# Kernel optimization log

Hardware: AMD Instinct MI355X
Metric: run time of the kernel (lower is better)

## Reference

```python
import jax, jax.numpy as jnp
import numpy as np

QUERY_DIM = 1024
CONTEXT_DIM = 768
HEADS = 16
DIM_HEAD = 64
INNER = HEADS * DIM_HEAD  # 1024
SCALE = DIM_HEAD ** -0.5


def setup_inputs() -> dict:
    key = jax.random.key(0)
    ks = jax.random.split(key, 8)
    b, nq, nkv = 4, 2048, 1024
    x = jax.random.normal(ks[0], (b, nq, QUERY_DIM), dtype=jnp.float32)
    context = jax.random.normal(ks[1], (b, nkv, CONTEXT_DIM), dtype=jnp.float32)
    mask = jax.random.randint(ks[2], (b, nkv), 0, 2).astype(jnp.bool_)
    s = 0.02
    Wq = jax.random.normal(ks[3], (QUERY_DIM, INNER), dtype=jnp.float32) * s
    Wk = jax.random.normal(ks[4], (CONTEXT_DIM, INNER), dtype=jnp.float32) * s
    Wv = jax.random.normal(ks[5], (CONTEXT_DIM, INNER), dtype=jnp.float32) * s
    Wo = jax.random.normal(ks[6], (INNER, QUERY_DIM), dtype=jnp.float32) * s
    bo = jnp.zeros((QUERY_DIM,), dtype=jnp.float32)
    return {"x": x, "context": context, "mask": mask,
            "Wq": Wq, "Wk": Wk, "Wv": Wv, "Wo": Wo, "bo": bo}


def reference(x, context, mask, Wq, Wk, Wv, Wo, bo):
    b, nq, _ = x.shape
    nkv = context.shape[1]
    h, d = HEADS, DIM_HEAD
    # QKV projections (no bias, as in nn.Linear(..., bias=False))
    q = (x @ Wq).reshape(b, nq, h, d).transpose(0, 2, 1, 3)       # [b,h,i,d]
    k = (context @ Wk).reshape(b, nkv, h, d).transpose(0, 2, 1, 3)  # [b,h,j,d]
    v = (context @ Wv).reshape(b, nkv, h, d).transpose(0, 2, 1, 3)  # [b,h,j,d]
    sim = jnp.einsum('bhid,bhjd->bhij', q, k) * SCALE
    # mask is per-key [b, j]; broadcast over heads and query positions
    neg = jnp.finfo(sim.dtype).min
    sim = jnp.where(mask[:, None, None, :], sim, neg)
    attn = jax.nn.softmax(sim, axis=-1)
    out = jnp.einsum('bhij,bhjd->bhid', attn, v)                  # [b,h,i,d]
    out = out.transpose(0, 2, 1, 3).reshape(b, nq, h * d)          # [b,i,hd]
    return out @ Wo + bo
```

## Files before the change

### kernel.cpp

```cpp
#include <hip/hip_runtime.h>

typedef unsigned short u16;
typedef __attribute__((ext_vector_type(8))) __bf16 bf16x8;
typedef __attribute__((ext_vector_type(4))) float f32x4;
typedef __attribute__((ext_vector_type(4))) u16 u16x4;

#define NB 4
#define NQ 2048
#define NKV 1024
#define NH 16
#define DH 64
#define DIN 1024
#define DCTX 768
#define NEGBIG -1e30f
#define QSC 0.180336881f

__device__ inline u16 f2bf(float f) {
  unsigned u = __builtin_bit_cast(unsigned, f);
  u += 0x7FFFu + ((u >> 16) & 1u);
  return (u16)(u >> 16);
}

__device__ inline unsigned cvtpk(float lo, float hi) {
  unsigned r;
  asm("v_cvt_pk_bf16_f32 %0, %1, %2" : "=v"(r) : "v"(lo), "v"(hi));
  return r;
}

__device__ inline float exp2a(float x) {
  float r;
  asm("v_exp_f32 %0, %1" : "=v"(r) : "v"(x));
  return r;
}

__global__ __launch_bounds__(256) void build_bias(const void* __restrict__ mask,
                                                  float* __restrict__ biasg) {
  __shared__ int notInt, notFloat;
  if (threadIdx.x == 0) { notInt = 0; notFloat = 0; }
  __syncthreads();
  const unsigned* mw = (const unsigned*)mask;
  int bad_i = 0, bad_f = 0;
#pragma unroll
  for (int e = 0; e < 4; e++) {
    unsigned v = mw[threadIdx.x * 4 + e];
    if (v > 1u) bad_i = 1;
    if (v != 0u && v != 0x3f800000u) bad_f = 1;
  }
  if (bad_i) atomicOr(&notInt, 1);
  if (bad_f) atomicOr(&notFloat, 1);
  __syncthreads();
  const int isInt = !notInt, isFloat = !notFloat;
  for (int i = threadIdx.x; i < NB * NKV; i += 256) {
    bool on;
    if (isInt)        on = ((const int*)mask)[i] != 0;
    else if (isFloat) on = ((const float*)mask)[i] != 0.f;
    else              on = ((const unsigned char*)mask)[i] != 0;
    biasg[i] = on ? 0.f : NEGBIG;
  }
}

__global__ __launch_bounds__(256) void cvt_bf16(const float* __restrict__ in,
                                                u16* __restrict__ out, int n) {
  int i = (blockIdx.x * 256 + threadIdx.x) * 4;
  if (i >= n) return;
  float4 v = *(const float4*)(in + i);
  u16x4 o = { f2bf(v.x), f2bf(v.y), f2bf(v.z), f2bf(v.w) };
  *(u16x4*)(out + i) = o;
}

__global__ __launch_bounds__(256) void transpose_cvt(const float* __restrict__ W,
                                                     u16* __restrict__ Wt, int K, int N) {
  __shared__ float tile[32][33];
  int n0 = blockIdx.x * 32, k0 = blockIdx.y * 32;
  int tx = threadIdx.x & 31, ty = threadIdx.x >> 5;
#pragma unroll
  for (int i = 0; i < 32; i += 8)
    tile[ty + i][tx] = W[(size_t)(k0 + ty + i) * N + n0 + tx];
  __syncthreads();
#pragma unroll
  for (int i = 0; i < 32; i += 8)
    Wt[(size_t)(n0 + ty + i) * K + k0 + tx] = f2bf(tile[tx][ty + i]);
}

__global__ __launch_bounds__(256) void vtrans(const u16* __restrict__ kvb, u16* __restrict__ vtg) {
  __shared__ __align__(16) u16 tile[64][72];
  const int t = threadIdx.x;
  const int jt = blockIdx.x, bh = blockIdx.y;
  const int b = bh >> 4, h = bh & 15;
  const int j0 = jt * 64;
  const int jl = t >> 2, c2 = t & 3;
  const u16* src = kvb + (size_t)(b * 1024 + j0 + jl) * 2048 + 1024 + h * 64 + c2 * 16;
  *(int4*)&tile[jl][c2 * 16]     = *(const int4*)(src);
  *(int4*)&tile[jl][c2 * 16 + 8] = *(const int4*)(src + 8);
  __syncthreads();
  const int dl = t >> 2;
  union { u16 e[16]; int4 q[2]; } pk;
#pragma unroll
  for (int e = 0; e < 16; e++) pk.e[e] = tile[c2 * 16 + e][dl];
  u16* dst = vtg + (size_t)(bh * 64 + dl) * 1024 + j0 + c2 * 16;
  *(int4*)dst       = pk.q[0];
  *(int4*)(dst + 8) = pk.q[1];
}

__global__ __launch_bounds__(256) void gemm_pipe(
    const u16* __restrict__ A0, const u16* __restrict__ B0, void* __restrict__ C0,
    const float* __restrict__ bias0, int N0, int K0, int mode0, int gx0,
    const u16* __restrict__ A1, const u16* __restrict__ B1, void* __restrict__ C1,
    const float* __restrict__ bias1, int N1, int K1, int mode1, int gx1, int split) {
  __shared__ __align__(16) u16 As[3 * 4096];
  __shared__ __align__(16) u16 Bs[3 * 4096];
  const u16 *A, *Bt; void* Cout; const float* bias;
  int N, K, mode, bx, by;
  {
    int bi = blockIdx.x;
    if (bi < split) { A = A0; Bt = B0; Cout = C0; bias = bias0; N = N0; K = K0; mode = mode0; bx = bi % gx0; by = bi / gx0; }
    else { bi -= split; A = A1; Bt = B1; Cout = C1; bias = bias1; N = N1; K = K1; mode = mode1; bx = bi % gx1; by = bi / gx1; }
  }
  const int t = threadIdx.x, w = t >> 6, l = t & 63, g = l >> 4, m16 = l & 15;
  const int brow = by * 128, bcol = bx * 128;
  const int wr = w >> 1, wc = w & 1;
  const int r_a = t >> 2;
  const int kb  = (t & 3) * 8;
  const int nk = K >> 5;
  f32x4 acc[4][4] = {};

#define G_STAGE(ks, bsel)                                                              \
  {                                                                                    \
    int k0_ = (ks) << 5;                                                               \
    _Pragma("unroll")                                                                  \
    for (int i = 0; i < 2; i++) {                                                      \
      const u16* ga = A + (size_t)(brow + i * 64 + r_a) * K + k0_ + kb;                \
      __builtin_amdgcn_global_load_lds(                                                \
          (const __attribute__((address_space(1))) void*)ga,                           \
          (__attribute__((address_space(3))) void*)((char*)As + (bsel) * 8192 + i * 4096 + w * 1024), \
          16, 0, 0);                                                                   \
      const u16* gb = Bt + (size_t)(bcol + i * 64 + r_a) * K + k0_ + kb;               \
      __builtin_amdgcn_global_load_lds(                                                \
          (const __attribute__((address_space(1))) void*)gb,                           \
          (__attribute__((address_space(3))) void*)((char*)Bs + (bsel) * 8192 + i * 4096 + w * 1024), \
          16, 0, 0);                                                                   \
    }                                                                                  \
  }

  G_STAGE(0, 0);
  G_STAGE(1, 1);
  int cur = 0, stg = 2;
  for (int ks = 0; ks < nk; ++ks) {
    if (ks + 1 < nk) asm volatile("s_waitcnt vmcnt(4)" ::: "memory");
    else             asm volatile("s_waitcnt vmcnt(0)" ::: "memory");
    asm volatile("s_barrier" ::: "memory");
    bf16x8 af[4], bfr[4];
#pragma unroll
    for (int m = 0; m < 4; m++)
      af[m] = *(const bf16x8*)(&As[cur * 4096 + (wr * 64 + m * 16 + m16) * 32 + g * 8]);
#pragma unroll
    for (int n = 0; n < 4; n++)
      bfr[n] = *(const bf16x8*)(&Bs[cur * 4096 + (wc * 64 + n * 16 + m16) * 32 + g * 8]);
    if (ks + 2 < nk) G_STAGE(ks + 2, stg);
#pragma unroll
    for (int m = 0; m < 4; m++)
#pragma unroll
      for (int n = 0; n < 4; n++)
        acc[m][n] = __builtin_amdgcn_mfma_f32_16x16x32_bf16(af[m], bfr[n], acc[m][n], 0, 0, 0);
    cur = (cur == 2) ? 0 : cur + 1;
    stg = (stg == 2) ? 0 : stg + 1;
  }
#undef G_STAGE

#pragma unroll
  for (int m = 0; m < 4; m++) {
    int grow = brow + wr * 64 + m * 16 + g * 4;
#pragma unroll
    for (int n = 0; n < 4; n++) {
      int gcol = bcol + wc * 64 + n * 16 + m16;
#pragma unroll
      for (int r = 0; r < 4; r++) {
        size_t off = (size_t)(grow + r) * N + gcol;
        if (mode == 0)      ((float*)Cout)[off] = acc[m][n][r] + bias[gcol];
        else if (mode == 1) ((u16*)Cout)[off] = f2bf(acc[m][n][r]);
        else                ((u16*)Cout)[off] = f2bf(acc[m][n][r] * QSC);
      }
    }
  }
}

__global__ __launch_bounds__(256) void attn(const u16* __restrict__ Q, const u16* __restrict__ Kb,
                                            const u16* __restrict__ Vt_g,
                                            const float* __restrict__ biasg,
                                            u16* __restrict__ O) {
  const int qt = blockIdx.x, h = blockIdx.y, b = blockIdx.z;
  const int t = threadIdx.x, w = t >> 6, l = t & 63, g = l >> 4, m16 = l & 15;
  const int bh = b * NH + h;

  __shared__ __align__(16) u16 Kl[2][4096];
  __shared__ __align__(16) u16 Vt[2][4096];
  __shared__ __align__(16) unsigned Pl[4][16 * 36];
  __shared__ float biasl[NKV];

  for (int i = t; i < NKV; i += 256) biasl[i] = biasg[(size_t)b * NKV + i];

  const int qrow = qt * 64 + w * 16 + m16;
  const u16* qp = Q + (size_t)(b * NQ + qrow) * DIN + h * DH;
  bf16x8 qA0 = *(const bf16x8*)(qp + g * 8);
  bf16x8 qA1 = *(const bf16x8*)(qp + 32 + g * 8);

  f32x4 oA[4] = {};
  float lA = 0.f;

#define STAGE_K(j0, bsel)                                                     \
  {                                                                           \
    _Pragma("unroll")                                                         \
    for (int n = 0; n < 2; n++) {                                             \
      int j_ = n * 32 + (t >> 3);                                             \
      int c_ = (t & 7) ^ (j_ & 7);                                            \
      const u16* gk = Kb + (size_t)(b * NKV + (j0) + j_) * 2048 + h * DH + c_ * 8; \
      __builtin_amdgcn_global_load_lds(                                       \
          (const __attribute__((address_space(1))) void*)gk,                  \
          (__attribute__((address_space(3))) void*)((char*)Kl + (bsel) * 8192 + n * 4096 + t * 16), \
          16, 0, 0);                                                          \
    }                                                                         \
  }
#define STAGE_V(j0, bsel)                                                     \
  {                                                                           \
    _Pragma("unroll")                                                         \
    for (int n = 0; n < 2; n++) {                                             \
      int d_ = n * 32 + (t >> 3);                                             \
      int c_ = (t & 7) ^ (d_ & 7);                                            \
      const u16* gv = Vt_g + (size_t)(bh * 64 + d_) * 1024 + (j0) + c_ * 8;   \
      __builtin_amdgcn_global_load_lds(                                       \
          (const __attribute__((address_space(1))) void*)gv,                  \
          (__attribute__((address_space(3))) void*)((char*)Vt + (bsel) * 8192 + n * 4096 + t * 16), \
          16, 0, 0);                                                          \
    }                                                                         \
  }

  STAGE_K(0, 0);
  STAGE_V(0, 0);
  asm volatile("s_waitcnt vmcnt(0) lgkmcnt(0)" ::: "memory");
  asm volatile("s_barrier" ::: "memory");

  for (int it = 0; it < 16; ++it) {
    const int cur = it & 1, nxt = cur ^ 1;
    const int j0 = it * 64;
    if (it + 1 < 16) {
      STAGE_K(j0 + 64, nxt);
      STAGE_V(j0 + 64, nxt);
    }

    f32x4 sA[4];
#pragma unroll
    for (int jt = 0; jt < 4; jt++) {
      int jr = jt * 16 + m16;
      const u16* krow = &Kl[cur][jr * 64];
      bf16x8 kf0 = *(const bf16x8*)(krow + ((g ^ (jr & 7)) * 8));
      bf16x8 kf1 = *(const bf16x8*)(krow + (((4 + g) ^ (jr & 7)) * 8));
      f32x4 z = {};
      f32x4 t0 = __builtin_amdgcn_mfma_f32_16x16x32_bf16(kf0, qA0, z, 0, 0, 0);
      sA[jt]   = __builtin_amdgcn_mfma_f32_16x16x32_bf16(kf1, qA1, t0, 0, 0, 0);
    }
    float4 b4[4];
#pragma unroll
    for (int jt = 0; jt < 4; jt++) b4[jt] = *(const float4*)&biasl[j0 + jt * 16 + g * 4];

    unsigned* plw = &Pl[w][0];
#pragma unroll
    for (int jt = 0; jt < 4; jt++) {
      float p0 = exp2a(sA[jt][0] + b4[jt].x);
      float p1 = exp2a(sA[jt][1] + b4[jt].y);
      float p2 = exp2a(sA[jt][2] + b4[jt].z);
      float p3 = exp2a(sA[jt][3] + b4[jt].w);
      lA += (p0 + p1) + (p2 + p3);
      uint2 u; u.x = cvtpk(p0, p1); u.y = cvtpk(p2, p3);
      *(uint2*)&plw[m16 * 36 + jt * 8 + 2 * g] = u;
    }
    asm volatile("" ::: "memory");
    bf16x8 pf0 = *(const bf16x8*)&plw[m16 * 36 + 4 * g];
    bf16x8 pf1 = *(const bf16x8*)&plw[m16 * 36 + 16 + 4 * g];
#pragma unroll
    for (int dt = 0; dt < 4; dt++) {
      int d = dt * 16 + m16;
      const u16* vrow = &Vt[cur][d * 64];
      bf16x8 vf0 = *(const bf16x8*)(vrow + ((g ^ (d & 7)) * 8));
      bf16x8 vf1 = *(const bf16x8*)(vrow + (((4 + g) ^ (d & 7)) * 8));
      oA[dt] = __builtin_amdgcn_mfma_f32_16x16x32_bf16(pf0, vf0, oA[dt], 0, 0, 0);
      oA[dt] = __builtin_amdgcn_mfma_f32_16x16x32_bf16(pf1, vf1, oA[dt], 0, 0, 0);
    }
    asm volatile("s_waitcnt vmcnt(0)" ::: "memory");
    asm volatile("s_barrier" ::: "memory");
  }
#undef STAGE_K
#undef STAGE_V

  lA += __shfl_xor(lA, 16); lA += __shfl_xor(lA, 32);
  float invA[4];
#pragma unroll
  for (int r = 0; r < 4; r++) invA[r] = 1.f / __shfl(lA, g * 4 + r);
  u16* op = O + (size_t)(b * NQ + qt * 64 + w * 16) * DIN + h * DH;
#pragma unroll
  for (int dt = 0; dt < 4; dt++)
#pragma unroll
    for (int r = 0; r < 4; r++)
      op[(size_t)(g * 4 + r) * DIN + dt * 16 + m16] = f2bf(oA[dt][r] * invA[r]);
}

extern "C" void kernel_launch(void* const* d_in, const int* in_sizes, int n_in,
                              void* d_out, int out_size, void* d_ws, size_t ws_size,
                              hipStream_t stream) {
  const float* x   = (const float*)d_in[0];
  const float* ctx = (const float*)d_in[1];
  const void*  mask = (const void*)d_in[2];
  const float* Wq  = (const float*)d_in[3];
  const float* Wk  = (const float*)d_in[4];
  const float* Wv  = (const float*)d_in[5];
  const float* Wo  = (const float*)d_in[6];
  const float* bo  = (const float*)d_in[7];
  float* out = (float*)d_out;

  char* ws = (char*)d_ws;
  u16* xb   = (u16*)(ws);
  u16* cb   = (u16*)(ws + 16777216);
  u16* wqt  = (u16*)(ws + 23068672);
  u16* wkv  = (u16*)(ws + 25165824);
  u16* wot  = (u16*)(ws + 28311552);
  u16* qb   = (u16*)(ws + 30408704);
  u16* kvb  = (u16*)(ws + 47185920);
  u16* vtg  = (u16*)(ws + 16777216);
  float* biasg = (float*)(ws + 63963136);
  u16* ab   = xb;

  build_bias<<<1, 256, 0, stream>>>(mask, biasg);
  cvt_bf16<<<8192, 256, 0, stream>>>(x, xb, 8388608);
  cvt_bf16<<<3072, 256, 0, stream>>>(ctx, cb, 3145728);
  transpose_cvt<<<dim3(32, 32), 256, 0, stream>>>(Wq, wqt, 1024, 1024);
  transpose_cvt<<<dim3(32, 24), 256, 0, stream>>>(Wk, wkv, 768, 1024);
  transpose_cvt<<<dim3(32, 24), 256, 0, stream>>>(Wv, wkv + 1024 * 768, 768, 1024);
  transpose_cvt<<<dim3(32, 32), 256, 0, stream>>>(Wo, wot, 1024, 1024);

  gemm_pipe<<<1024, 256, 0, stream>>>(
      xb, wqt, qb, nullptr, 1024, 1024, 2, 8,
      cb, wkv, kvb, nullptr, 2048, 768, 1, 16, 512);

  vtrans<<<dim3(16, 64), 256, 0, stream>>>(kvb, vtg);

  attn<<<dim3(32, 16, 4), 256, 0, stream>>>(qb, kvb, vtg, biasg, ab);

  gemm_pipe<<<512, 256, 0, stream>>>(
      ab, wot, out, bo, 1024, 1024, 0, 8,
      ab, wot, out, bo, 1024, 1024, 0, 8, 512);
}
```

Before: 290.0 us.

## Replace 128x128 GEMM with 256x128, BK=64, swizzled double-buffered 512-thread kernel

Swaps the merged 128x128x32 triple-buffered GEMM for a 256x128 tile with K-step 64, run by 8 waves of 512 threads. The larger tile is meant to raise operand reuse per LDS load. An XOR swizzle on the LDS layout is meant to avoid bank conflicts on the wider 64-element rows. The pipeline drops from three stages to two, with a full vmcnt(0) wait each iteration, and the Q and KV projections now run as two separate launches. In exchange, each GEMM has fewer blocks, about one per CU, which can hurt latency hiding and load balance.

```diff
diff --git a/kernel.cpp b/kernel.cpp
--- a/kernel.cpp
+++ b/kernel.cpp
@@ -102,70 +102,73 @@
   *(int4*)(dst + 8) = pk.q[1];
 }
 
-__global__ __launch_bounds__(256) void gemm_pipe(
-    const u16* __restrict__ A0, const u16* __restrict__ B0, void* __restrict__ C0,
-    const float* __restrict__ bias0, int N0, int K0, int mode0, int gx0,
-    const u16* __restrict__ A1, const u16* __restrict__ B1, void* __restrict__ C1,
-    const float* __restrict__ bias1, int N1, int K1, int mode1, int gx1, int split) {
-  __shared__ __align__(16) u16 As[3 * 4096];
-  __shared__ __align__(16) u16 Bs[3 * 4096];
-  const u16 *A, *Bt; void* Cout; const float* bias;
-  int N, K, mode, bx, by;
-  {
-    int bi = blockIdx.x;
-    if (bi < split) { A = A0; Bt = B0; Cout = C0; bias = bias0; N = N0; K = K0; mode = mode0; bx = bi % gx0; by = bi / gx0; }
-    else { bi -= split; A = A1; Bt = B1; Cout = C1; bias = bias1; N = N1; K = K1; mode = mode1; bx = bi % gx1; by = bi / gx1; }
-  }
+__global__ __launch_bounds__(512) void gemm256(const u16* __restrict__ A,
+                                               const u16* __restrict__ Bt,
+                                               void* __restrict__ Cout,
+                                               const float* __restrict__ bias,
+                                               int N, int K, int mode) {
+  __shared__ __align__(16) u16 As[2][256 * 64];
+  __shared__ __align__(16) u16 Bs[2][128 * 64];
   const int t = threadIdx.x, w = t >> 6, l = t & 63, g = l >> 4, m16 = l & 15;
-  const int brow = by * 128, bcol = bx * 128;
+  const int brow = blockIdx.y * 256, bcol = blockIdx.x * 128;
   const int wr = w >> 1, wc = w & 1;
-  const int r_a = t >> 2;
-  const int kb  = (t & 3) * 8;
-  const int nk = K >> 5;
+  const int nk = K >> 6;
+  const int srow = t >> 3;
+  const int sc   = t & 7;
   f32x4 acc[4][4] = {};
 
-#define G_STAGE(ks, bsel)                                                              \
-  {                                                                                    \
-    int k0_ = (ks) << 5;                                                               \
-    _Pragma("unroll")                                                                  \
-    for (int i = 0; i < 2; i++) {                                                      \
-      const u16* ga = A + (size_t)(brow + i * 64 + r_a) * K + k0_ + kb;                \
-      __builtin_amdgcn_global_load_lds(                                                \
-          (const __attribute__((address_space(1))) void*)ga,                           \
-          (__attribute__((address_space(3))) void*)((char*)As + (bsel) * 8192 + i * 4096 + w * 1024), \
-          16, 0, 0);                                                                   \
-      const u16* gb = Bt + (size_t)(bcol + i * 64 + r_a) * K + k0_ + kb;               \
-      __builtin_amdgcn_global_load_lds(                                                \
-          (const __attribute__((address_space(1))) void*)gb,                           \
-          (__attribute__((address_space(3))) void*)((char*)Bs + (bsel) * 8192 + i * 4096 + w * 1024), \
-          16, 0, 0);                                                                   \
-    }                                                                                  \
-  }
-
-  G_STAGE(0, 0);
-  G_STAGE(1, 1);
-  int cur = 0, stg = 2;
+#define STAGE(ks, bsel)                                                              \
+  {                                                                                  \
+    int k0_ = (ks) << 6;                                                             \
+    _Pragma("unroll")                                                                \
+    for (int r = 0; r < 4; r++) {                                                    \
+      int row = r * 64 + srow;                                                       \
+      int cs = sc ^ (row & 7);                                                       \
+      const u16* ga = A + (size_t)(brow + row) * K + k0_ + cs * 8;                   \
+      __builtin_amdgcn_global_load_lds(                                              \
+          (const __attribute__((address_space(1))) void*)ga,                         \
+          (__attribute__((address_space(3))) void*)((char*)As + (bsel) * 32768 + r * 8192 + t * 16), \
+          16, 0, 0);                                                                 \
+    }                                                                                \
+    _Pragma("unroll")                                                                \
+    for (int r = 0; r < 2; r++) {                                                    \
+      int row = r * 64 + srow;                                                       \
+      int cs = sc ^ (row & 7);                                                       \
+      const u16* gb = Bt + (size_t)(bcol + row) * K + k0_ + cs * 8;                  \
+      __builtin_amdgcn_global_load_lds(                                              \
+          (const __attribute__((address_space(1))) void*)gb,                         \
+          (__attribute__((address_space(3))) void*)((char*)Bs + (bsel) * 16384 + r * 8192 + t * 16), \
+          16, 0, 0);                                                                 \
+    }                                                                                \
+  }
+
+  STAGE(0, 0);
+  asm volatile("s_waitcnt vmcnt(0)" ::: "memory");
+  asm volatile("s_barrier" ::: "memory");
+
   for (int ks = 0; ks < nk; ++ks) {
-    if (ks + 1 < nk) asm volatile("s_waitcnt vmcnt(4)" ::: "memory");
-    else             asm volatile("s_waitcnt vmcnt(0)" ::: "memory");
+    const int cur = ks & 1;
+    if (ks + 1 < nk) STAGE(ks + 1, cur ^ 1);
+#pragma unroll
+    for (int kh = 0; kh < 2; kh++) {
+      bf16x8 af[4], bfr[4];
+      const int cp = ((kh * 4 + g) ^ (m16 & 7)) * 8;
+#pragma unroll
+      for (int m = 0; m < 4; m++)
+        af[m] = *(const bf16x8*)(&As[cur][(wr * 64 + m * 16 + m16) * 64 + cp]);
+#pragma unroll
+      for (int n = 0; n < 4; n++)
+        bfr[n] = *(const bf16x8*)(&Bs[cur][(wc * 64 + n * 16 + m16) * 64 + cp]);
+#pragma unroll
+      for (int m = 0; m < 4; m++)
+#pragma unroll
+        for (int n = 0; n < 4; n++)
+          acc[m][n] = __builtin_amdgcn_mfma_f32_16x16x32_bf16(af[m], bfr[n], acc[m][n], 0, 0, 0);
+    }
+    asm volatile("s_waitcnt vmcnt(0)" ::: "memory");
     asm volatile("s_barrier" ::: "memory");
-    bf16x8 af[4], bfr[4];
-#pragma unroll
-    for (int m = 0; m < 4; m++)
-      af[m] = *(const bf16x8*)(&As[cur * 4096 + (wr * 64 + m * 16 + m16) * 32 + g * 8]);
-#pragma unroll
-    for (int n = 0; n < 4; n++)
-      bfr[n] = *(const bf16x8*)(&Bs[cur * 4096 + (wc * 64 + n * 16 + m16) * 32 + g * 8]);
-    if (ks + 2 < nk) G_STAGE(ks + 2, stg);
-#pragma unroll
-    for (int m = 0; m < 4; m++)
-#pragma unroll
-      for (int n = 0; n < 4; n++)
-        acc[m][n] = __builtin_amdgcn_mfma_f32_16x16x32_bf16(af[m], bfr[n], acc[m][n], 0, 0, 0);
-    cur = (cur == 2) ? 0 : cur + 1;
-    stg = (stg == 2) ? 0 : stg + 1;
-  }
-#undef G_STAGE
+  }
+#undef STAGE
 
 #pragma unroll
   for (int m = 0; m < 4; m++) {
@@ -336,15 +339,12 @@
   transpose_cvt<<<dim3(32, 24), 256, 0, stream>>>(Wv, wkv + 1024 * 768, 768, 1024);
   transpose_cvt<<<dim3(32, 32), 256, 0, stream>>>(Wo, wot, 1024, 1024);
 
-  gemm_pipe<<<1024, 256, 0, stream>>>(
-      xb, wqt, qb, nullptr, 1024, 1024, 2, 8,
-      cb, wkv, kvb, nullptr, 2048, 768, 1, 16, 512);
+  gemm256<<<dim3(8, 32), 512, 0, stream>>>(xb, wqt, qb, nullptr, 1024, 1024, 2);
+  gemm256<<<dim3(16, 16), 512, 0, stream>>>(cb, wkv, kvb, nullptr, 2048, 768, 1);
 
   vtrans<<<dim3(16, 64), 256, 0, stream>>>(kvb, vtg);
 
   attn<<<dim3(32, 16, 4), 256, 0, stream>>>(qb, kvb, vtg, biasg, ab);
 
-  gemm_pipe<<<512, 256, 0, stream>>>(
-      ab, wot, out, bo, 1024, 1024, 0, 8,
-      ab, wot, out, bo, 1024, 1024, 0, 8, 512);
-}
+  gemm256<<<dim3(8, 32), 512, 0, stream>>>(ab, wot, out, bo, 1024, 1024, 0);
+}
```

Result: slower. 295.8 us (+2.0%).
